# Performance work log

Measured on AMD Instinct MI355X. Metric: run time of the kernel, lower is better.

## Reference

```python
import jax, jax.numpy as jnp
import numpy as np

V, H, B, S, J, T, NOP = 30000, 512, 16, 256, 10, 8, 4
NEG = -1e9


def setup_inputs() -> dict:
    key = jax.random.key(0)
    ks = jax.random.split(key, 10)
    return {
        "x": jax.random.randint(ks[0], (B, S), 0, V),
        "encoder_output": jax.random.normal(ks[1], (B, S, H), jnp.float32),
        "encoder_hidden": jax.random.normal(ks[2], (B, H), jnp.float32),
        "max_len": T,
        "emb_W": jax.random.normal(ks[3], (V, H), jnp.float32) * 0.02,
        "slot_emb": jax.random.normal(ks[4], (J, H), jnp.float32) * 0.1,
        "W_ih": jax.random.normal(ks[5], (3 * H, H), jnp.float32) * 0.02,
        "W_hh": jax.random.normal(ks[6], (3 * H, H), jnp.float32) * 0.02,
        "b_ih": jnp.zeros((3 * H,), jnp.float32),
        "b_hh": jnp.zeros((3 * H,), jnp.float32),
        "w_gen_W": jax.random.normal(ks[7], (1, 3 * H), jnp.float32) * 0.02,
        "w_gen_b": jnp.zeros((1,), jnp.float32),
        "action_W": jax.random.normal(ks[8], (NOP, H), jnp.float32) * 0.02,
        "action_b": jnp.zeros((NOP,), jnp.float32),
    }


def gru_step(xin, h, W_ih, W_hh, b_ih, b_hh):
    # xin, h: (J, B, H). PyTorch GRU gate order: r, z, n.
    gi = xin @ W_ih.T + b_ih
    gh = h @ W_hh.T + b_hh
    ir, iz, inn = jnp.split(gi, 3, axis=-1)
    hr, hz, hn = jnp.split(gh, 3, axis=-1)
    r = jax.nn.sigmoid(ir + hr)
    z = jax.nn.sigmoid(iz + hz)
    n = jnp.tanh(inn + r * hn)
    return (1.0 - z) * n + z * h


def reference(x, encoder_output, encoder_hidden, max_len, emb_W, slot_emb,
              W_ih, W_hh, b_ih, b_hh, w_gen_W, w_gen_b, action_W, action_b):
    nJ, nH = slot_emb.shape
    nB, nS = x.shape
    nV = emb_W.shape[0]
    mask = (x == 0)  # (B, S) pad mask
    xJ = jnp.broadcast_to(x[None], (nJ, nB, nS))
    jidx = jnp.arange(nJ)[:, None, None]
    bidx = jnp.arange(nB)[None, :, None]

    w0 = jnp.broadcast_to(slot_emb[:, None, :], (nJ, nB, nH))  # slot query per slot
    h0 = jnp.broadcast_to(encoder_hidden[None], (nJ, nB, nH))

    def step(carry, _):
        w, h = carry
        h = gru_step(w, h, W_ih, W_hh, b_ih, b_hh)
        # attention over encoder states
        attn_e = jnp.einsum('bsh,jbh->jbs', encoder_output, h)
        attn_e = jnp.where(mask[None], NEG, attn_e)
        attn_hist = jax.nn.softmax(attn_e, axis=-1)          # (J,B,S)
        context = jnp.einsum('jbs,bsh->jbh', attn_hist, encoder_output)
        # vocab distribution
        attn_vocab = jax.nn.softmax(h @ emb_W.T, axis=-1)    # (J,B,V)
        # pointer-generator mix
        gen_in = jnp.concatenate([w, h, context], axis=-1)   # (J,B,3H)
        p_gen = jax.nn.sigmoid(gen_in @ w_gen_W.T + w_gen_b) # (J,B,1)
        p_ctx = jnp.zeros((nJ, nB, nV), attn_vocab.dtype).at[jidx, bidx, xJ].add(attn_hist)
        p_final = p_gen * attn_vocab + (1.0 - p_gen) * p_ctx # (J,B,V)
        w_idx = jnp.argmax(p_final, axis=-1)                 # greedy next token
        w_next = emb_W[w_idx]                                # (J,B,H)
        return (w_next, h), (p_final, context)

    (_, _), (p_all, ctx_all) = jax.lax.scan(step, (w0, h0), None, length=max_len)
    # gate head uses context from first decode step (k == 0)
    gates = ctx_all[0] @ action_W.T + action_b               # (J,B,n_op)
    all_gate = jnp.transpose(gates, (1, 0, 2))               # (B,J,n_op)
    all_point = jnp.transpose(p_all, (2, 1, 0, 3))           # (B,J,T,V)
    return all_gate, all_point
```

## Files before the change

### kernel.cpp

```cpp
#include <hip/hip_runtime.h>
#include <math.h>

#define V 30000
#define H 512
#define NB 16
#define NS 256
#define NJ 10
#define NT 8
#define NOPS 4
#define NR 160
#define EV 30720
#define NEGV -1e9f

typedef __attribute__((ext_vector_type(8))) short short8;
typedef __attribute__((ext_vector_type(4))) short short4v;
typedef __attribute__((ext_vector_type(4))) float f32x4;

__device__ inline float bf2f(unsigned short s) {
    union { unsigned int u; float f; } c; c.u = ((unsigned int)s) << 16;
    return c.f;
}
__device__ inline unsigned short f2bf(float f) {
    union { float f; unsigned int u; } c; c.f = f;
    unsigned int u = c.u;
    u += 0x7fffu + ((u >> 16) & 1u);
    return (unsigned short)(u >> 16);
}
__device__ inline unsigned long long packkey(float f, int v) {
    union { float f; unsigned int u; } c; c.f = f;
    return ((unsigned long long)c.u << 32) | (unsigned int)(0x7FFFFFFF - v);
}

__global__ void k_setup_emb(const float* __restrict__ emb, unsigned short* __restrict__ emb_bf, int n8) {
    int gid = blockIdx.x * 256 + threadIdx.x;
    if (gid >= n8) return;
    const float4* src = (const float4*)emb + (size_t)gid * 2;
    float4 a = src[0], b = src[1];
    short8 o;
    o[0] = (short)f2bf(a.x); o[1] = (short)f2bf(a.y); o[2] = (short)f2bf(a.z); o[3] = (short)f2bf(a.w);
    o[4] = (short)f2bf(b.x); o[5] = (short)f2bf(b.y); o[6] = (short)f2bf(b.z); o[7] = (short)f2bf(b.w);
    *(short8*)(emb_bf + (size_t)gid * 8) = o;
}

__global__ void k_setup_small(const float* __restrict__ Wih, const float* __restrict__ Whh,
    unsigned short* wih_hi, unsigned short* wih_lo, unsigned short* whh_hi, unsigned short* whh_lo,
    const float* __restrict__ slot, const float* __restrict__ ench,
    float* w_g, unsigned short* w_hi, unsigned short* w_lo,
    float* h_g, unsigned short* h_hi, unsigned short* h_lo)
{
    int gid = blockIdx.x * 256 + threadIdx.x;
    if (gid < 786432) {
        float v1 = Wih[gid];
        unsigned short hi = f2bf(v1);
        wih_hi[gid] = hi; wih_lo[gid] = f2bf(v1 - bf2f(hi));
        float v2 = Whh[gid];
        hi = f2bf(v2);
        whh_hi[gid] = hi; whh_lo[gid] = f2bf(v2 - bf2f(hi));
    } else {
        int i = gid - 786432;
        if (i < NR * H) {
            int jb = i >> 9, d = i & 511;
            int j = jb >> 4, b = jb & 15;
            float wv = slot[j * H + d];
            w_g[i] = wv;
            unsigned short hi = f2bf(wv);
            w_hi[i] = hi; w_lo[i] = f2bf(wv - bf2f(hi));
            float hv = ench[b * H + d];
            h_g[i] = hv;
            hi = f2bf(hv);
            h_hi[i] = hi; h_lo[i] = f2bf(hv - bf2f(hi));
        }
    }
}

#define GRU_APAD 520
__global__ __launch_bounds__(256) void k_gru_gemm(
    const unsigned short* __restrict__ w_hi, const unsigned short* __restrict__ w_lo,
    const unsigned short* __restrict__ h_hi, const unsigned short* __restrict__ h_lo,
    const unsigned short* __restrict__ wih_hi, const unsigned short* __restrict__ wih_lo,
    const unsigned short* __restrict__ whh_hi, const unsigned short* __restrict__ whh_lo,
    float* __restrict__ gi, float* __restrict__ gh)
{
    __shared__ unsigned short Ah[16 * GRU_APAD];
    __shared__ unsigned short Al[16 * GRU_APAD];
    int nch = blockIdx.x, mt = blockIdx.y, z = blockIdx.z;
    const unsigned short* Asrc_hi = z ? h_hi : w_hi;
    const unsigned short* Asrc_lo = z ? h_lo : w_lo;
    const unsigned short* Bhi = z ? whh_hi : wih_hi;
    const unsigned short* Blo = z ? whh_lo : wih_lo;
    float* outp = z ? gh : gi;
    int t = threadIdx.x;
    for (int i = t; i < 2048; i += 256) {
        int matl = i >> 10;
        int row = (i >> 6) & 15;
        int seg = i & 63;
        const unsigned short* src = (matl ? Asrc_lo : Asrc_hi) + (mt * 16 + row) * 512 + seg * 8;
        unsigned short* dst = (matl ? Al : Ah) + row * GRU_APAD + seg * 8;
        *(short8*)dst = *(const short8*)src;
    }
    __syncthreads();
    int wv = t >> 6, lane = t & 63;
    int col15 = lane & 15, quad = lane >> 4;
    f32x4 acc0 = {0.f, 0.f, 0.f, 0.f}, acc1 = {0.f, 0.f, 0.f, 0.f};
    int c0 = nch * 128 + wv * 32 + col15;
    int c1 = c0 + 16;
    const unsigned short* bhp0 = Bhi + c0 * 512 + quad * 8;
    const unsigned short* bhp1 = Bhi + c1 * 512 + quad * 8;
    const unsigned short* blp0 = Blo + c0 * 512 + quad * 8;
    const unsigned short* blp1 = Blo + c1 * 512 + quad * 8;
    const unsigned short* ahp = Ah + col15 * GRU_APAD + quad * 8;
    const unsigned short* alp = Al + col15 * GRU_APAD + quad * 8;
#pragma unroll
    for (int ks = 0; ks < 16; ks++) {
        int ko = ks * 32;
        short8 bh0 = *(const short8*)(bhp0 + ko);
        short8 bh1 = *(const short8*)(bhp1 + ko);
        short8 bl0 = *(const short8*)(blp0 + ko);
        short8 bl1 = *(const short8*)(blp1 + ko);
        short8 ah = *(const short8*)(ahp + ko);
        short8 al = *(const short8*)(alp + ko);
        acc0 = __builtin_amdgcn_mfma_f32_16x16x32_bf16(ah, bh0, acc0, 0, 0, 0);
        acc1 = __builtin_amdgcn_mfma_f32_16x16x32_bf16(ah, bh1, acc1, 0, 0, 0);
        acc0 = __builtin_amdgcn_mfma_f32_16x16x32_bf16(ah, bl0, acc0, 0, 0, 0);
        acc1 = __builtin_amdgcn_mfma_f32_16x16x32_bf16(ah, bl1, acc1, 0, 0, 0);
        acc0 = __builtin_amdgcn_mfma_f32_16x16x32_bf16(al, bh0, acc0, 0, 0, 0);
        acc1 = __builtin_amdgcn_mfma_f32_16x16x32_bf16(al, bh1, acc1, 0, 0, 0);
    }
#pragma unroll
    for (int r = 0; r < 4; r++) {
        int row = mt * 16 + quad * 4 + r;
        outp[row * 1536 + c0] = acc0[r];
        outp[row * 1536 + c1] = acc1[r];
    }
}

__global__ __launch_bounds__(256) void k_attention(
    const float* __restrict__ gi, const float* __restrict__ gh,
    const float* __restrict__ b_ih, const float* __restrict__ b_hh,
    float* __restrict__ h_g, unsigned short* __restrict__ h_hi, unsigned short* __restrict__ h_lo,
    const float* __restrict__ enc, const int* __restrict__ x,
    const float* __restrict__ w_g, const float* __restrict__ wgenW, const float* __restrict__ wgenb,
    float* __restrict__ attn_g, float* __restrict__ pgen_g,
    float* __restrict__ ctx0, int store_ctx,
    float* __restrict__ rowsum, unsigned long long* __restrict__ argpk)
{
    __shared__ float h_lds[512];
    __shared__ float sc[256];
    __shared__ float red[256];
    __shared__ float ctxp[4 * 512];
    int jb = blockIdx.x;
    int b = jb & 15;
    int t = threadIdx.x;
    if (t == 0) { rowsum[jb] = 0.f; argpk[jb] = 0ull; }
    for (int d = t; d < 512; d += 256) {
        int base = jb * 1536;
        float ir = gi[base + d]        + b_ih[d];
        float iz = gi[base + 512 + d]  + b_ih[512 + d];
        float in = gi[base + 1024 + d] + b_ih[1024 + d];
        float hr = gh[base + d]        + b_hh[d];
        float hz = gh[base + 512 + d]  + b_hh[512 + d];
        float hn = gh[base + 1024 + d] + b_hh[1024 + d];
        float hold = h_g[jb * 512 + d];
        float r = 1.f / (1.f + expf(-(ir + hr)));
        float z = 1.f / (1.f + expf(-(iz + hz)));
        float n = tanhf(in + r * hn);
        float hnew = (1.f - z) * n + z * hold;
        h_lds[d] = hnew;
        h_g[jb * 512 + d] = hnew;
        unsigned short hi = f2bf(hnew);
        h_hi[jb * 512 + d] = hi;
        h_lo[jb * 512 + d] = f2bf(hnew - bf2f(hi));
    }
    __syncthreads();
    int wid = t >> 6, lane = t & 63;
    float hreg[8];
#pragma unroll
    for (int i = 0; i < 8; i++) hreg[i] = h_lds[lane * 8 + i];
    const float* encb = enc + (size_t)b * NS * H;
    for (int s = wid; s < NS; s += 4) {
        const float4* er = (const float4*)(encb + s * 512 + lane * 8);
        float4 e0 = er[0], e1 = er[1];
        float p = e0.x * hreg[0] + e0.y * hreg[1] + e0.z * hreg[2] + e0.w * hreg[3]
                + e1.x * hreg[4] + e1.y * hreg[5] + e1.z * hreg[6] + e1.w * hreg[7];
#pragma unroll
        for (int off = 32; off > 0; off >>= 1) p += __shfl_down(p, off);
        if (lane == 0) sc[s] = (x[b * NS + s] == 0) ? NEGV : p;
    }
    __syncthreads();
    red[t] = sc[t];
    __syncthreads();
    for (int sft = 128; sft > 0; sft >>= 1) { if (t < sft) red[t] = fmaxf(red[t], red[t + sft]); __syncthreads(); }
    float m = red[0];
    __syncthreads();
    float e = expf(sc[t] - m);
    red[t] = e;
    __syncthreads();
    for (int sft = 128; sft > 0; sft >>= 1) { if (t < sft) red[t] += red[t + sft]; __syncthreads(); }
    float inv = 1.f / red[0];
    float p_s = e * inv;
    sc[t] = p_s;
    attn_g[jb * NS + t] = p_s;
    __syncthreads();
    {
        float cp[8] = {0.f,0.f,0.f,0.f,0.f,0.f,0.f,0.f};
        const float* encw = encb + lane * 8;
        for (int s = wid * 64; s < wid * 64 + 64; s++) {
            float ps = sc[s];
            const float4* er = (const float4*)(encw + s * 512);
            float4 e0 = er[0], e1 = er[1];
            cp[0] += ps * e0.x; cp[1] += ps * e0.y; cp[2] += ps * e0.z; cp[3] += ps * e0.w;
            cp[4] += ps * e1.x; cp[5] += ps * e1.y; cp[6] += ps * e1.z; cp[7] += ps * e1.w;
        }
        float* cw = ctxp + wid * 512 + lane * 8;
#pragma unroll
        for (int i = 0; i < 8; i++) cw[i] = cp[i];
    }
    __syncthreads();
    int d0 = 2 * t, d1 = 2 * t + 1;
    float c0 = ctxp[d0] + ctxp[512 + d0] + ctxp[1024 + d0] + ctxp[1536 + d0];
    float c1 = ctxp[d1] + ctxp[512 + d1] + ctxp[1024 + d1] + ctxp[1536 + d1];
    if (store_ctx) ((float2*)ctx0)[jb * 256 + t] = make_float2(c0, c1);
    float pg = wgenW[d0] * w_g[jb * 512 + d0] + wgenW[d1] * w_g[jb * 512 + d1]
             + wgenW[512 + d0] * h_lds[d0] + wgenW[512 + d1] * h_lds[d1]
             + wgenW[1024 + d0] * c0 + wgenW[1024 + d1] * c1;
    __syncthreads();
    red[t] = pg;
    __syncthreads();
    for (int sft = 128; sft > 0; sft >>= 1) { if (t < sft) red[t] += red[t + sft]; __syncthreads(); }
    if (t == 0) pgen_g[jb] = 1.f / (1.f + expf(-(red[0] + wgenb[0])));
}

#define VPAD 136
__global__ __launch_bounds__(256) void k_vgemm(
    const unsigned short* __restrict__ h_hi, const unsigned short* __restrict__ emb_bf,
    unsigned short* __restrict__ E, float* __restrict__ rowsum,
    unsigned long long* __restrict__ argpk)
{
    __shared__ unsigned short A[160 * VPAD];
    int blk = blockIdx.x;
    int t = threadIdx.x;
    int wv = t >> 6, lane = t & 63, col15 = lane & 15, quad = lane >> 4;
    int v = blk * 128 + wv * 32 + col15;
    f32x4 acc[10][2];
#pragma unroll
    for (int m = 0; m < 10; m++) {
        acc[m][0] = (f32x4){0.f, 0.f, 0.f, 0.f};
        acc[m][1] = (f32x4){0.f, 0.f, 0.f, 0.f};
    }
    int v0c = min(v, V - 1);
    int v1c = min(v + 16, V - 1);
    for (int kc = 0; kc < 4; kc++) {
        __syncthreads();
        for (int i = t; i < 2560; i += 256) {
            int row = i >> 4, seg = i & 15;
            *(short8*)(A + row * VPAD + seg * 8) = *(const short8*)(h_hi + row * 512 + kc * 128 + seg * 8);
        }
        __syncthreads();
#pragma unroll
        for (int ks = 0; ks < 4; ks++) {
            int kl = ks * 32 + quad * 8;
            int kg = kc * 128 + kl;
            short8 b0 = *(const short8*)(emb_bf + (size_t)v0c * 512 + kg);
            short8 b1 = *(const short8*)(emb_bf + (size_t)v1c * 512 + kg);
#pragma unroll
            for (int m = 0; m < 10; m++) {
                short8 a = *(const short8*)(A + (m * 16 + col15) * VPAD + kl);
                acc[m][0] = __builtin_amdgcn_mfma_f32_16x16x32_bf16(a, b0, acc[m][0], 0, 0, 0);
                acc[m][1] = __builtin_amdgcn_mfma_f32_16x16x32_bf16(a, b1, acc[m][1], 0, 0, 0);
            }
        }
    }
    __syncthreads();
#pragma unroll
    for (int m = 0; m < 10; m++) {
#pragma unroll
        for (int tile = 0; tile < 2; tile++) {
            int vv = v + tile * 16;
            int cl = wv * 32 + tile * 16 + col15;
#pragma unroll
            for (int r = 0; r < 4; r++) {
                int row = m * 16 + quad * 4 + r;
                float ev = (vv < V) ? expf(acc[m][tile][r]) : 0.f;
                A[row * VPAD + cl] = f2bf(ev);
            }
        }
    }
    __syncthreads();
    if (t < 160) {
        float s = 0.f;
        unsigned long long key = 0ull;
#pragma unroll
        for (int seg = 0; seg < 16; seg++) {
            short8 ev = *(const short8*)(A + t * VPAD + seg * 8);
#pragma unroll
            for (int k = 0; k < 8; k++) {
                float f = bf2f((unsigned short)ev[k]);
                s += f;
                unsigned long long kk = packkey(f, blk * 128 + seg * 8 + k);
                key = (kk > key) ? kk : key;
            }
        }
        atomicAdd(rowsum + t, s);
        atomicMax(argpk + t, key);
    }
    {
        int rsub = t >> 4, seg = t & 15;
        for (int it = 0; it < 10; it++) {
            int row = it * 16 + rsub;
            short8 ev = *(const short8*)(A + row * VPAD + seg * 8);
            *(short8*)(E + (size_t)row * EV + blk * 128 + seg * 8) = ev;
        }
    }
}

__global__ __launch_bounds__(256) void k_finalize(
    const unsigned short* __restrict__ E, const float* __restrict__ pgen_g,
    const float* __restrict__ rowsum, const unsigned long long* __restrict__ argpk,
    const float* __restrict__ attn_g, const int* __restrict__ x,
    const float* __restrict__ emb, float* __restrict__ out,
    float* __restrict__ w_g, unsigned short* __restrict__ w_hi, unsigned short* __restrict__ w_lo,
    const float* __restrict__ ctx0, const float* __restrict__ aW, const float* __restrict__ ab,
    int tstep)
{
    __shared__ float bvs[256];
    __shared__ int bis[256];
    __shared__ float red[256];
    int jb = blockIdx.x, t = threadIdx.x;
    int j = jb >> 4, b = jb & 15;
    float inv = 1.f / rowsum[jb];
    float pgen = pgen_g[jb];
    float scale = pgen * inv;
    const unsigned short* Er = E + (size_t)jb * EV;
    size_t outbase = (size_t)640 + ((size_t)(b * NJ + j) * NT + tstep) * V;
    float* op = out + outbase;
    for (int c = 0; c < 29; c++) {
        int vv = c * 1024 + t * 4;
        short4v e = *(const short4v*)(Er + vv);
        float4 p = make_float4(bf2f((unsigned short)e[0]) * scale, bf2f((unsigned short)e[1]) * scale,
                               bf2f((unsigned short)e[2]) * scale, bf2f((unsigned short)e[3]) * scale);
        *(float4*)(op + vv) = p;
    }
    if (t < 76) {
        int vv = 29696 + t * 4;
        short4v e = *(const short4v*)(Er + vv);
        float4 p = make_float4(bf2f((unsigned short)e[0]) * scale, bf2f((unsigned short)e[1]) * scale,
                               bf2f((unsigned short)e[2]) * scale, bf2f((unsigned short)e[3]) * scale);
        *(float4*)(op + vv) = p;
    }
    __syncthreads();
    float best; int besti;
    {
        int vv = x[b * NS + t];
        float a = (1.f - pgen) * attn_g[jb * NS + t];
        float old = atomicAdd(&op[vv], a);
        best = old + a;
        besti = vv;
    }
    bvs[t] = best; bis[t] = besti;
    __syncthreads();
    for (int sft = 128; sft > 0; sft >>= 1) {
        if (t < sft) {
            if (bvs[t + sft] > bvs[t] || (bvs[t + sft] == bvs[t] && bis[t + sft] < bis[t])) {
                bvs[t] = bvs[t + sft]; bis[t] = bis[t + sft];
            }
        }
        __syncthreads();
    }
    int widx;
    {
        unsigned long long key = argpk[jb];
        union { unsigned int u; float f; } c; c.u = (unsigned int)(key >> 32);
        float db = c.f * scale;
        int di = 0x7FFFFFFF - (int)(key & 0xFFFFFFFFu);
        float sb = bvs[0]; int si = bis[0];
        widx = (sb > db || (sb == db && si < di)) ? si : di;
    }
    for (int d = t; d < 512; d += 256) {
        float val = emb[(size_t)widx * 512 + d];
        w_g[jb * 512 + d] = val;
        unsigned short hi = f2bf(val);
        w_hi[jb * 512 + d] = hi;
        w_lo[jb * 512 + d] = f2bf(val - bf2f(hi));
    }
    if (tstep == 0) {
        float part[4] = {0.f, 0.f, 0.f, 0.f};
        for (int d = t; d < 512; d += 256) {
            float c = ctx0[jb * 512 + d];
#pragma unroll
            for (int o = 0; o < 4; o++) part[o] += c * aW[o * 512 + d];
        }
        for (int o = 0; o < 4; o++) {
            __syncthreads();
            red[t] = part[o];
            __syncthreads();
            for (int sft = 128; sft > 0; sft >>= 1) { if (t < sft) red[t] += red[t + sft]; __syncthreads(); }
            if (t == 0) out[(b * NJ + j) * NOPS + o] = red[0] + ab[o];
        }
    }
}

extern "C" void kernel_launch(void* const* d_in, const int* in_sizes, int n_in,
                              void* d_out, int out_size, void* d_ws, size_t ws_size,
                              hipStream_t stream) {
    const int*   x     = (const int*)d_in[0];
    const float* enc   = (const float*)d_in[1];
    const float* ench  = (const float*)d_in[2];
    const float* embW  = (const float*)d_in[4];
    const float* slot  = (const float*)d_in[5];
    const float* Wih   = (const float*)d_in[6];
    const float* Whh   = (const float*)d_in[7];
    const float* bih   = (const float*)d_in[8];
    const float* bhh   = (const float*)d_in[9];
    const float* wgenW = (const float*)d_in[10];
    const float* wgenb = (const float*)d_in[11];
    const float* aW    = (const float*)d_in[12];
    const float* ab    = (const float*)d_in[13];
    float* out = (float*)d_out;

    char* ws = (char*)d_ws;
    size_t off = 0;
    auto carve = [&](size_t bytes) { char* p = ws + off; off += (bytes + 255) & ~(size_t)255; return p; };
    unsigned short* emb_bf = (unsigned short*)carve((size_t)V * H * 2);
    unsigned short* wih_hi = (unsigned short*)carve(786432 * 2);
    unsigned short* wih_lo = (unsigned short*)carve(786432 * 2);
    unsigned short* whh_hi = (unsigned short*)carve(786432 * 2);
    unsigned short* whh_lo = (unsigned short*)carve(786432 * 2);
    float* w_f32 = (float*)carve(NR * H * 4);
    float* h_f32 = (float*)carve(NR * H * 4);
    float* ctx0  = (float*)carve(NR * H * 4);
    unsigned short* w_hi = (unsigned short*)carve(NR * H * 2);
    unsigned short* w_lo = (unsigned short*)carve(NR * H * 2);
    unsigned short* h_hi = (unsigned short*)carve(NR * H * 2);
    unsigned short* h_lo = (unsigned short*)carve(NR * H * 2);
    float* gi   = (float*)carve(NR * 1536 * 4);
    float* gh   = (float*)carve(NR * 1536 * 4);
    float* attn = (float*)carve(NR * NS * 4);
    float* pgen = (float*)carve(NR * 4);
    float* rowsum = (float*)carve(NR * 4);
    unsigned long long* argpk = (unsigned long long*)carve(NR * 8);
    unsigned short* E = (unsigned short*)carve((size_t)NR * EV * 2);

    k_setup_emb<<<7500, 256, 0, stream>>>(embW, emb_bf, (V * H) / 8);
    k_setup_small<<<3392, 256, 0, stream>>>(Wih, Whh, wih_hi, wih_lo, whh_hi, whh_lo,
                                            slot, ench, w_f32, w_hi, w_lo, h_f32, h_hi, h_lo);
    for (int t = 0; t < NT; t++) {
        k_gru_gemm<<<dim3(12, 10, 2), 256, 0, stream>>>(w_hi, w_lo, h_hi, h_lo,
                                                        wih_hi, wih_lo, whh_hi, whh_lo, gi, gh);
        k_attention<<<NR, 256, 0, stream>>>(gi, gh, bih, bhh, h_f32, h_hi, h_lo, enc, x,
                                            w_f32, wgenW, wgenb, attn, pgen, ctx0, t == 0 ? 1 : 0,
                                            rowsum, argpk);
        k_vgemm<<<240, 256, 0, stream>>>(h_hi, emb_bf, E, rowsum, argpk);
        k_finalize<<<NR, 256, 0, stream>>>(E, pgen, rowsum, argpk, attn, x, embW, out,
                                           w_f32, w_hi, w_lo, ctx0, aW, ab, t);
    }
}
```

Baseline: 1.102 ms.

## Fuse per-step decode kernels into one persistent cooperative kernel with grid syncs

```diff
diff --git a/kernel.cpp b/kernel.cpp
--- a/kernel.cpp
+++ b/kernel.cpp
@@ -1,5 +1,8 @@
 #include <hip/hip_runtime.h>
+#include <hip/hip_cooperative_groups.h>
 #include <math.h>
+
+namespace cg = cooperative_groups;
 
 #define V 30000
 #define H 512
@@ -73,22 +76,36 @@
     }
 }
 
+struct DecArgs {
+    const int* x;
+    const float* enc;
+    const float* embW;
+    const float* bih; const float* bhh;
+    const float* wgenW; const float* wgenb;
+    const float* aW; const float* ab;
+    const unsigned short* emb_bf;
+    const unsigned short* wih_hi; const unsigned short* wih_lo;
+    const unsigned short* whh_hi; const unsigned short* whh_lo;
+    float* w_g; float* h_g; float* ctx0;
+    unsigned short* w_hi; unsigned short* w_lo;
+    unsigned short* h_hi; unsigned short* h_lo;
+    float* gi; float* gh;
+    float* attn; float* pgen;
+    float* rowsum; unsigned long long* argpk;
+    unsigned short* E;
+    float* out;
+};
+
 #define GRU_APAD 520
-__global__ __launch_bounds__(256) void k_gru_gemm(
-    const unsigned short* __restrict__ w_hi, const unsigned short* __restrict__ w_lo,
-    const unsigned short* __restrict__ h_hi, const unsigned short* __restrict__ h_lo,
-    const unsigned short* __restrict__ wih_hi, const unsigned short* __restrict__ wih_lo,
-    const unsigned short* __restrict__ whh_hi, const unsigned short* __restrict__ whh_lo,
-    float* __restrict__ gi, float* __restrict__ gh)
-{
-    __shared__ unsigned short Ah[16 * GRU_APAD];
-    __shared__ unsigned short Al[16 * GRU_APAD];
-    int nch = blockIdx.x, mt = blockIdx.y, z = blockIdx.z;
-    const unsigned short* Asrc_hi = z ? h_hi : w_hi;
-    const unsigned short* Asrc_lo = z ? h_lo : w_lo;
-    const unsigned short* Bhi = z ? whh_hi : wih_hi;
-    const unsigned short* Blo = z ? whh_lo : wih_lo;
-    float* outp = z ? gh : gi;
+__device__ void phase_gru(int task, const DecArgs& P, unsigned char* smem) {
+    unsigned short* Ah = (unsigned short*)smem;
+    unsigned short* Al = (unsigned short*)(smem + 16640);
+    int nch = task % 12, mt = (task / 12) % 10, z = task / 120;
+    const unsigned short* Asrc_hi = z ? P.h_hi : P.w_hi;
+    const unsigned short* Asrc_lo = z ? P.h_lo : P.w_lo;
+    const unsigned short* Bhi = z ? P.whh_hi : P.wih_hi;
+    const unsigned short* Blo = z ? P.whh_lo : P.wih_lo;
+    float* outp = z ? P.gh : P.gi;
     int t = threadIdx.x;
     for (int i = t; i < 2048; i += 256) {
         int matl = i >> 10;
@@ -134,49 +151,39 @@
     }
 }
 
-__global__ __launch_bounds__(256) void k_attention(
-    const float* __restrict__ gi, const float* __restrict__ gh,
-    const float* __restrict__ b_ih, const float* __restrict__ b_hh,
-    float* __restrict__ h_g, unsigned short* __restrict__ h_hi, unsigned short* __restrict__ h_lo,
-    const float* __restrict__ enc, const int* __restrict__ x,
-    const float* __restrict__ w_g, const float* __restrict__ wgenW, const float* __restrict__ wgenb,
-    float* __restrict__ attn_g, float* __restrict__ pgen_g,
-    float* __restrict__ ctx0, int store_ctx,
-    float* __restrict__ rowsum, unsigned long long* __restrict__ argpk)
-{
-    __shared__ float h_lds[512];
-    __shared__ float sc[256];
-    __shared__ float red[256];
-    __shared__ float ctxp[4 * 512];
-    int jb = blockIdx.x;
+__device__ void phase_attention(int jb, const DecArgs& P, unsigned char* smem, int store_ctx) {
+    float* h_lds = (float*)smem;
+    float* sc    = (float*)(smem + 2048);
+    float* red   = (float*)(smem + 3072);
+    float* ctxp  = (float*)(smem + 4096);
     int b = jb & 15;
     int t = threadIdx.x;
-    if (t == 0) { rowsum[jb] = 0.f; argpk[jb] = 0ull; }
+    if (t == 0) { P.rowsum[jb] = 0.f; P.argpk[jb] = 0ull; }
     for (int d = t; d < 512; d += 256) {
         int base = jb * 1536;
-        float ir = gi[base + d]        + b_ih[d];
-        float iz = gi[base + 512 + d]  + b_ih[512 + d];
-        float in = gi[base + 1024 + d] + b_ih[1024 + d];
-        float hr = gh[base + d]        + b_hh[d];
-        float hz = gh[base + 512 + d]  + b_hh[512 + d];
-        float hn = gh[base + 1024 + d] + b_hh[1024 + d];
-        float hold = h_g[jb * 512 + d];
+        float ir = P.gi[base + d]        + P.bih[d];
+        float iz = P.gi[base + 512 + d]  + P.bih[512 + d];
+        float in = P.gi[base + 1024 + d] + P.bih[1024 + d];
+        float hr = P.gh[base + d]        + P.bhh[d];
+        float hz = P.gh[base + 512 + d]  + P.bhh[512 + d];
+        float hn = P.gh[base + 1024 + d] + P.bhh[1024 + d];
+        float hold = P.h_g[jb * 512 + d];
         float r = 1.f / (1.f + expf(-(ir + hr)));
         float z = 1.f / (1.f + expf(-(iz + hz)));
         float n = tanhf(in + r * hn);
         float hnew = (1.f - z) * n + z * hold;
         h_lds[d] = hnew;
-        h_g[jb * 512 + d] = hnew;
+        P.h_g[jb * 512 + d] = hnew;
         unsigned short hi = f2bf(hnew);
-        h_hi[jb * 512 + d] = hi;
-        h_lo[jb * 512 + d] = f2bf(hnew - bf2f(hi));
+        P.h_hi[jb * 512 + d] = hi;
+        P.h_lo[jb * 512 + d] = f2bf(hnew - bf2f(hi));
     }
     __syncthreads();
     int wid = t >> 6, lane = t & 63;
     float hreg[8];
 #pragma unroll
     for (int i = 0; i < 8; i++) hreg[i] = h_lds[lane * 8 + i];
-    const float* encb = enc + (size_t)b * NS * H;
+    const float* encb = P.enc + (size_t)b * NS * H;
     for (int s = wid; s < NS; s += 4) {
         const float4* er = (const float4*)(encb + s * 512 + lane * 8);
         float4 e0 = er[0], e1 = er[1];
@@ -184,7 +191,7 @@
                 + e1.x * hreg[4] + e1.y * hreg[5] + e1.z * hreg[6] + e1.w * hreg[7];
 #pragma unroll
         for (int off = 32; off > 0; off >>= 1) p += __shfl_down(p, off);
-        if (lane == 0) sc[s] = (x[b * NS + s] == 0) ? NEGV : p;
+        if (lane == 0) sc[s] = (P.x[b * NS + s] == 0) ? NEGV : p;
     }
     __syncthreads();
     red[t] = sc[t];
@@ -199,7 +206,7 @@
     float inv = 1.f / red[0];
     float p_s = e * inv;
     sc[t] = p_s;
-    attn_g[jb * NS + t] = p_s;
+    P.attn[jb * NS + t] = p_s;
     __syncthreads();
     {
         float cp[8] = {0.f,0.f,0.f,0.f,0.f,0.f,0.f,0.f};
@@ -219,25 +226,20 @@
     int d0 = 2 * t, d1 = 2 * t + 1;
     float c0 = ctxp[d0] + ctxp[512 + d0] + ctxp[1024 + d0] + ctxp[1536 + d0];
     float c1 = ctxp[d1] + ctxp[512 + d1] + ctxp[1024 + d1] + ctxp[1536 + d1];
-    if (store_ctx) ((float2*)ctx0)[jb * 256 + t] = make_float2(c0, c1);
-    float pg = wgenW[d0] * w_g[jb * 512 + d0] + wgenW[d1] * w_g[jb * 512 + d1]
-             + wgenW[512 + d0] * h_lds[d0] + wgenW[512 + d1] * h_lds[d1]
-             + wgenW[1024 + d0] * c0 + wgenW[1024 + d1] * c1;
+    if (store_ctx) ((float2*)P.ctx0)[jb * 256 + t] = make_float2(c0, c1);
+    float pg = P.wgenW[d0] * P.w_g[jb * 512 + d0] + P.wgenW[d1] * P.w_g[jb * 512 + d1]
+             + P.wgenW[512 + d0] * h_lds[d0] + P.wgenW[512 + d1] * h_lds[d1]
+             + P.wgenW[1024 + d0] * c0 + P.wgenW[1024 + d1] * c1;
     __syncthreads();
     red[t] = pg;
     __syncthreads();
     for (int sft = 128; sft > 0; sft >>= 1) { if (t < sft) red[t] += red[t + sft]; __syncthreads(); }
-    if (t == 0) pgen_g[jb] = 1.f / (1.f + expf(-(red[0] + wgenb[0])));
+    if (t == 0) P.pgen[jb] = 1.f / (1.f + expf(-(red[0] + P.wgenb[0])));
 }
 
 #define VPAD 136
-__global__ __launch_bounds__(256) void k_vgemm(
-    const unsigned short* __restrict__ h_hi, const unsigned short* __restrict__ emb_bf,
-    unsigned short* __restrict__ E, float* __restrict__ rowsum,
-    unsigned long long* __restrict__ argpk)
-{
-    __shared__ unsigned short A[160 * VPAD];
-    int blk = blockIdx.x;
+__device__ void phase_vgemm(int blk, const DecArgs& P, unsigned char* smem) {
+    unsigned short* A = (unsigned short*)smem;
     int t = threadIdx.x;
     int wv = t >> 6, lane = t & 63, col15 = lane & 15, quad = lane >> 4;
     int v = blk * 128 + wv * 32 + col15;
@@ -253,15 +255,15 @@
         __syncthreads();
         for (int i = t; i < 2560; i += 256) {
             int row = i >> 4, seg = i & 15;
-            *(short8*)(A + row * VPAD + seg * 8) = *(const short8*)(h_hi + row * 512 + kc * 128 + seg * 8);
+            *(short8*)(A + row * VPAD + seg * 8) = *(const short8*)(P.h_hi + row * 512 + kc * 128 + seg * 8);
         }
         __syncthreads();
 #pragma unroll
         for (int ks = 0; ks < 4; ks++) {
             int kl = ks * 32 + quad * 8;
             int kg = kc * 128 + kl;
-            short8 b0 = *(const short8*)(emb_bf + (size_t)v0c * 512 + kg);
-            short8 b1 = *(const short8*)(emb_bf + (size_t)v1c * 512 + kg);
+            short8 b0 = *(const short8*)(P.emb_bf + (size_t)v0c * 512 + kg);
+            short8 b1 = *(const short8*)(P.emb_bf + (size_t)v1c * 512 + kg);
 #pragma unroll
             for (int m = 0; m < 10; m++) {
                 short8 a = *(const short8*)(A + (m * 16 + col15) * VPAD + kl);
@@ -300,39 +302,31 @@
                 key = (kk > key) ? kk : key;
             }
         }
-        atomicAdd(rowsum + t, s);
-        atomicMax(argpk + t, key);
+        atomicAdd(P.rowsum + t, s);
+        atomicMax(P.argpk + t, key);
     }
     {
         int rsub = t >> 4, seg = t & 15;
         for (int it = 0; it < 10; it++) {
             int row = it * 16 + rsub;
             short8 ev = *(const short8*)(A + row * VPAD + seg * 8);
-            *(short8*)(E + (size_t)row * EV + blk * 128 + seg * 8) = ev;
-        }
-    }
-}
-
-__global__ __launch_bounds__(256) void k_finalize(
-    const unsigned short* __restrict__ E, const float* __restrict__ pgen_g,
-    const float* __restrict__ rowsum, const unsigned long long* __restrict__ argpk,
-    const float* __restrict__ attn_g, const int* __restrict__ x,
-    const float* __restrict__ emb, float* __restrict__ out,
-    float* __restrict__ w_g, unsigned short* __restrict__ w_hi, unsigned short* __restrict__ w_lo,
-    const float* __restrict__ ctx0, const float* __restrict__ aW, const float* __restrict__ ab,
-    int tstep)
-{
-    __shared__ float bvs[256];
-    __shared__ int bis[256];
-    __shared__ float red[256];
-    int jb = blockIdx.x, t = threadIdx.x;
+            *(short8*)(P.E + (size_t)row * EV + blk * 128 + seg * 8) = ev;
+        }
+    }
+}
+
+__device__ void phase_finalize(int jb, const DecArgs& P, unsigned char* smem, int tstep) {
+    float* bvs = (float*)smem;
+    int* bis   = (int*)(smem + 1024);
+    float* red = (float*)(smem + 2048);
+    int t = threadIdx.x;
     int j = jb >> 4, b = jb & 15;
-    float inv = 1.f / rowsum[jb];
-    float pgen = pgen_g[jb];
+    float inv = 1.f / P.rowsum[jb];
+    float pgen = P.pgen[jb];
     float scale = pgen * inv;
-    const unsigned short* Er = E + (size_t)jb * EV;
+    const unsigned short* Er = P.E + (size_t)jb * EV;
     size_t outbase = (size_t)640 + ((size_t)(b * NJ + j) * NT + tstep) * V;
-    float* op = out + outbase;
+    float* op = P.out + outbase;
     for (int c = 0; c < 29; c++) {
         int vv = c * 1024 + t * 4;
         short4v e = *(const short4v*)(Er + vv);
@@ -350,8 +344,8 @@
     __syncthreads();
     float best; int besti;
     {
-        int vv = x[b * NS + t];
-        float a = (1.f - pgen) * attn_g[jb * NS + t];
+        int vv = P.x[b * NS + t];
+        float a = (1.f - pgen) * P.attn[jb * NS + t];
         float old = atomicAdd(&op[vv], a);
         best = old + a;
         besti = vv;
@@ -368,7 +362,7 @@
     }
     int widx;
     {
-        unsigned long long key = argpk[jb];
+        unsigned long long key = P.argpk[jb];
         union { unsigned int u; float f; } c; c.u = (unsigned int)(key >> 32);
         float db = c.f * scale;
         int di = 0x7FFFFFFF - (int)(key & 0xFFFFFFFFu);
@@ -376,26 +370,42 @@
         widx = (sb > db || (sb == db && si < di)) ? si : di;
     }
     for (int d = t; d < 512; d += 256) {
-        float val = emb[(size_t)widx * 512 + d];
-        w_g[jb * 512 + d] = val;
+        float val = P.embW[(size_t)widx * 512 + d];
+        P.w_g[jb * 512 + d] = val;
         unsigned short hi = f2bf(val);
-        w_hi[jb * 512 + d] = hi;
-        w_lo[jb * 512 + d] = f2bf(val - bf2f(hi));
+        P.w_hi[jb * 512 + d] = hi;
+        P.w_lo[jb * 512 + d] = f2bf(val - bf2f(hi));
     }
     if (tstep == 0) {
         float part[4] = {0.f, 0.f, 0.f, 0.f};
         for (int d = t; d < 512; d += 256) {
-            float c = ctx0[jb * 512 + d];
-#pragma unroll
-            for (int o = 0; o < 4; o++) part[o] += c * aW[o * 512 + d];
+            float c = P.ctx0[jb * 512 + d];
+#pragma unroll
+            for (int o = 0; o < 4; o++) part[o] += c * P.aW[o * 512 + d];
         }
         for (int o = 0; o < 4; o++) {
             __syncthreads();
             red[t] = part[o];
             __syncthreads();
             for (int sft = 128; sft > 0; sft >>= 1) { if (t < sft) red[t] += red[t + sft]; __syncthreads(); }
-            if (t == 0) out[(b * NJ + j) * NOPS + o] = red[0] + ab[o];
-        }
+            if (t == 0) P.out[(b * NJ + j) * NOPS + o] = red[0] + P.ab[o];
+        }
+    }
+}
+
+__global__ __launch_bounds__(256, 2) void k_decode(DecArgs P) {
+    cg::grid_group grid = cg::this_grid();
+    __shared__ __align__(16) unsigned char smem[43520];
+    int blk = blockIdx.x;
+    for (int t = 0; t < NT; t++) {
+        if (blk < 240) phase_gru(blk, P, smem);
+        grid.sync();
+        if (blk < 160) phase_attention(blk, P, smem, t == 0 ? 1 : 0);
+        grid.sync();
+        if (blk < 240) phase_vgemm(blk, P, smem);
+        grid.sync();
+        if (blk < 160) phase_finalize(blk, P, smem, t);
+        grid.sync();
     }
 }
 
@@ -443,14 +453,18 @@
     k_setup_emb<<<7500, 256, 0, stream>>>(embW, emb_bf, (V * H) / 8);
     k_setup_small<<<3392, 256, 0, stream>>>(Wih, Whh, wih_hi, wih_lo, whh_hi, whh_lo,
                                             slot, ench, w_f32, w_hi, w_lo, h_f32, h_hi, h_lo);
-    for (int t = 0; t < NT; t++) {
-        k_gru_gemm<<<dim3(12, 10, 2), 256, 0, stream>>>(w_hi, w_lo, h_hi, h_lo,
-                                                        wih_hi, wih_lo, whh_hi, whh_lo, gi, gh);
-        k_attention<<<NR, 256, 0, stream>>>(gi, gh, bih, bhh, h_f32, h_hi, h_lo, enc, x,
-                                            w_f32, wgenW, wgenb, attn, pgen, ctx0, t == 0 ? 1 : 0,
-                                            rowsum, argpk);
-        k_vgemm<<<240, 256, 0, stream>>>(h_hi, emb_bf, E, rowsum, argpk);
-        k_finalize<<<NR, 256, 0, stream>>>(E, pgen, rowsum, argpk, attn, x, embW, out,
-                                           w_f32, w_hi, w_lo, ctx0, aW, ab, t);
-    }
-}
+
+    DecArgs P;
+    P.x = x; P.enc = enc; P.embW = embW;
+    P.bih = bih; P.bhh = bhh; P.wgenW = wgenW; P.wgenb = wgenb;
+    P.aW = aW; P.ab = ab;
+    P.emb_bf = emb_bf;
+    P.wih_hi = wih_hi; P.wih_lo = wih_lo; P.whh_hi = whh_hi; P.whh_lo = whh_lo;
+    P.w_g = w_f32; P.h_g = h_f32; P.ctx0 = ctx0;
+    P.w_hi = w_hi; P.w_lo = w_lo; P.h_hi = h_hi; P.h_lo = h_lo;
+    P.gi = gi; P.gh = gh; P.attn = attn; P.pgen = pgen;
+    P.rowsum = rowsum; P.argpk = argpk; P.E = E; P.out = out;
+
+    void* kargs[] = { (void*)&P };
+    (void)hipLaunchCooperativeKernel((const void*)k_decode, dim3(240), dim3(256), kargs, 0, stream);
+}
```

Measured after the change: 2.265 ms. 106% more time.
